# Performance work log

Hardware: AMD Instinct MI355X
Metric: run time of the kernel (lower is better)

Reference implementation:

```python
import jax, jax.numpy as jnp
import numpy as np

# Dimensions
B, T, S, V, CV, D = 32, 128, 400, 32000, 600, 512
PAD = 1  # vocabs['code'].stoi['<blank>']


def setup_inputs() -> dict:
    key = jax.random.key(0)
    k0, k1, k2, k3, k4 = jax.random.split(key, 5)
    hidden = jax.random.normal(k0, (B * T, D), dtype=jnp.float32)
    # attention weights: normalized over source length
    copy_attn = jax.nn.softmax(jax.random.normal(k1, (B * T, S), dtype=jnp.float32), axis=-1)
    # src_map: one-hot scatter matrix [B, S, CV] mapping src positions to extended-vocab ids
    src_ids = jax.random.randint(k2, (B, S), 0, CV)
    src_map = jax.nn.one_hot(src_ids, CV, dtype=jnp.float32)
    W = jax.random.normal(k3, (V, D), dtype=jnp.float32) * 0.02
    b = jnp.zeros((V,), dtype=jnp.float32)
    w_copy = jax.random.normal(k4, (D,), dtype=jnp.float32) * 0.02
    b_copy = jnp.zeros((), dtype=jnp.float32)
    return {"hidden": hidden, "copy_attn": copy_attn, "src_map": src_map,
            "W": W, "b": b, "w_copy": w_copy, "b_copy": b_copy}


def reference(hidden, copy_attn, src_map, W, b, w_copy, b_copy):
    # logits over target vocab, pad logit masked to -inf
    logits = hidden @ W.T + b                      # [B*T, V]
    logits = logits.at[:, PAD].set(-jnp.inf)
    prob = jax.nn.softmax(logits, axis=-1)         # [B*T, V]
    # copy gate p(z)
    copy = jax.nn.sigmoid(hidden @ w_copy + b_copy)[:, None]  # [B*T, 1]
    out_prob = prob * (1.0 - copy)                 # generation branch
    mul_attn = copy_attn * copy                    # copy branch, [B*T, S]
    # scatter attention mass into extended vocab via one-hot bmm
    copy_prob = jnp.einsum('bts,bsv->btv', mul_attn.reshape(B, T, S), src_map)
    copy_prob = copy_prob.reshape(-1, src_map.shape[-1])  # [B*T, CV]
    return jnp.concatenate([out_prob, copy_prob], axis=1)  # [B*T, V+CV]
```

## Files before the change

kernel.cpp:

```cpp
#include <hip/hip_runtime.h>
#include <hip/hip_bf16.h>
#include <cstdint>
#include <cstddef>

#define M_ROWS   4096
#define N_VOCAB  32000
#define K_DIM    512
#define S_DIM    400
#define CV_DIM   600
#define OUT_PITCH 32600
#define PAD_IDX  1

typedef __attribute__((ext_vector_type(8))) short short8;
typedef __attribute__((ext_vector_type(8))) unsigned short ushort8;
typedef __attribute__((ext_vector_type(4))) float f32x4;

#define WB_OFF   0ull
#define HB_OFF   32768000ull
#define COPYG_OFF 36962304ull
#define RSUM_OFF  36978688ull
#define SSCALE_OFF 36995072ull
#define SRCID_OFF 37011456ull
#define EB_OFF    37062656ull
#define WS_NEED_BF16 (EB_OFF + 262144000ull)

__device__ inline void gload_lds16(const void* g, void* l) {
  __builtin_amdgcn_global_load_lds(
      (const __attribute__((address_space(1))) unsigned int*)g,
      (__attribute__((address_space(3))) unsigned int*)l, 16, 0, 0);
}

__device__ inline unsigned short f32_to_bf16_rn(float f) {
  unsigned u = __float_as_uint(f);
  u += 0x7FFFu + ((u >> 16) & 1u);
  return (unsigned short)(u >> 16);
}
__device__ inline float bf16_to_f32(unsigned short h) {
  return __uint_as_float((unsigned)h << 16);
}

__global__ void cvt_kernel(const float4* __restrict__ in, ushort4* __restrict__ out, unsigned n4) {
  unsigned stride = gridDim.x * blockDim.x;
  for (unsigned i = blockIdx.x * blockDim.x + threadIdx.x; i < n4; i += stride) {
    float4 v = in[i];
    ushort4 o;
    o.x = f32_to_bf16_rn(v.x);
    o.y = f32_to_bf16_rn(v.y);
    o.z = f32_to_bf16_rn(v.z);
    o.w = f32_to_bf16_rn(v.w);
    out[i] = o;
  }
}

__global__ void copygate_cvt_kernel(const float* __restrict__ hidden,
                                    const float* __restrict__ w_copy,
                                    const float* __restrict__ b_copy,
                                    float* __restrict__ copyg,
                                    unsigned short* __restrict__ Hb) {
  unsigned gw = (blockIdx.x * blockDim.x + threadIdx.x) >> 6;
  unsigned lane = threadIdx.x & 63u;
  if (gw >= M_ROWS) return;
  const float4* h4 = (const float4*)(hidden + (size_t)gw * K_DIM);
  const float4* w4 = (const float4*)w_copy;
  float4 a0 = h4[lane * 2 + 0], w0 = w4[lane * 2 + 0];
  float4 a1 = h4[lane * 2 + 1], w1 = w4[lane * 2 + 1];
  float dot = a0.x * w0.x + a0.y * w0.y + a0.z * w0.z + a0.w * w0.w
            + a1.x * w1.x + a1.y * w1.y + a1.z * w1.z + a1.w * w1.w;
  ushort8 hb;
  hb[0] = f32_to_bf16_rn(a0.x); hb[1] = f32_to_bf16_rn(a0.y);
  hb[2] = f32_to_bf16_rn(a0.z); hb[3] = f32_to_bf16_rn(a0.w);
  hb[4] = f32_to_bf16_rn(a1.x); hb[5] = f32_to_bf16_rn(a1.y);
  hb[6] = f32_to_bf16_rn(a1.z); hb[7] = f32_to_bf16_rn(a1.w);
  *(ushort8*)(Hb + (size_t)gw * K_DIM + lane * 8u) = hb;
  #pragma unroll
  for (int mask = 1; mask < 64; mask <<= 1) dot += __shfl_xor(dot, mask);
  if (lane == 0) copyg[gw] = 1.f / (1.f + __expf(-(dot + b_copy[0])));
}

__global__ void srcids_kernel(const float* __restrict__ src_map, int* __restrict__ src_ids) {
  unsigned pos = (blockIdx.x * blockDim.x + threadIdx.x) >> 6;
  unsigned lane = threadIdx.x & 63u;
  if (pos >= 32 * S_DIM) return;
  const float* row = src_map + (size_t)pos * CV_DIM;
  int found = 1 << 30;
  for (int v = lane; v < CV_DIM; v += 64)
    if (row[v] > 0.5f) found = v;
  #pragma unroll
  for (int mask = 1; mask < 64; mask <<= 1) {
    int o = __shfl_xor(found, mask);
    found = found < o ? found : o;
  }
  if (lane == 0) src_ids[pos] = found;
}

template<int BF16OUT>
__global__ __launch_bounds__(512, 2)
void gemm_exp_kernel(const unsigned short* __restrict__ A,
                     const unsigned short* __restrict__ B,
                     const float* __restrict__ bias,
                     float* __restrict__ out,
                     unsigned short* __restrict__ Eb,
                     float* __restrict__ row_sum) {
  __shared__ unsigned short smem[24576];
  unsigned short* As = smem;
  unsigned short* Bs = smem + 16384;

  unsigned bid = blockIdx.x;
  unsigned xcd = bid & 7u, local = bid >> 3;
  unsigned slab = xcd >> 1, half = xcd & 1u;
  unsigned nt = half * 125u + (local >> 2);
  unsigned mt = slab * 4u + (local & 3u);
  unsigned m0 = mt * 256u, n0 = nt * 128u;

  unsigned tid = threadIdx.x;
  unsigned lane = tid & 63u;
  unsigned wid = tid >> 6;
  unsigned wm = wid >> 1, wn = wid & 1u;
  unsigned lr = lane >> 4, lc = lane & 15u;

  const unsigned ch0 = (lr ^ (lc & 7u)) * 8u;
  const unsigned ch1 = ((lr + 4u) ^ (lc & 7u)) * 8u;

  const unsigned short* Asrc[4];
  const unsigned short* Bsrc[2];
  unsigned dstA[4], dstB[2];
  #pragma unroll
  for (unsigned i = 0; i < 4; ++i) {
    unsigned u = i * 512u + tid;
    unsigned rr = u >> 3;
    unsigned ch = (u & 7u) ^ (rr & 7u);
    dstA[i] = u * 16u;
    Asrc[i] = A + (size_t)(m0 + rr) * K_DIM + ch * 8u;
  }
  #pragma unroll
  for (unsigned i = 0; i < 2; ++i) {
    unsigned u = i * 512u + tid;
    unsigned rr = u >> 3;
    unsigned ch = (u & 7u) ^ (rr & 7u);
    dstB[i] = u * 16u;
    Bsrc[i] = B + (size_t)(n0 + rr) * K_DIM + ch * 8u;
  }
  unsigned arow[4], brow[4];
  #pragma unroll
  for (int m = 0; m < 4; ++m) arow[m] = (wm * 64u + m * 16u + lc) * 64u;
  #pragma unroll
  for (int n = 0; n < 4; ++n) brow[n] = 16384u + (wn * 64u + n * 16u + lc) * 64u;

  f32x4 acc[4][4] = {};

  for (unsigned kt = 0; kt < 8; ++kt) {
    unsigned k0 = kt * 64u;
    #pragma unroll
    for (unsigned i = 0; i < 4; ++i)
      gload_lds16(Asrc[i] + k0, (char*)As + dstA[i]);
    #pragma unroll
    for (unsigned i = 0; i < 2; ++i)
      gload_lds16(Bsrc[i] + k0, (char*)smem + 32768u + dstB[i]);
    __syncthreads();
    {
      short8 af[4][2], bf[4][2];
      #pragma unroll
      for (int m = 0; m < 4; ++m) {
        af[m][0] = *(const short8*)&As[arow[m] + ch0];
        af[m][1] = *(const short8*)&As[arow[m] + ch1];
      }
      #pragma unroll
      for (int n = 0; n < 4; ++n) {
        bf[n][0] = *(const short8*)&smem[brow[n] + ch0];
        bf[n][1] = *(const short8*)&smem[brow[n] + ch1];
      }
      #pragma unroll
      for (int ks = 0; ks < 2; ++ks)
        #pragma unroll
        for (int m = 0; m < 4; ++m)
          #pragma unroll
          for (int n = 0; n < 4; ++n)
            acc[m][n] = __builtin_amdgcn_mfma_f32_16x16x32_bf16(bf[n][ks], af[m][ks],
                                                                acc[m][n], 0, 0, 0);
    }
    __syncthreads();
  }

  float4 bv4[4];
  #pragma unroll
  for (int n = 0; n < 4; ++n)
    bv4[n] = *(const float4*)&bias[n0 + wn * 64u + n * 16u + lr * 4u];

  if (BF16OUT) {
    #pragma unroll
    for (int m = 0; m < 4; ++m) {
      unsigned grow = m0 + wm * 64u + m * 16u + lc;
      unsigned short* rowp = Eb + (size_t)grow * N_VOCAB;
      #pragma unroll
      for (int n = 0; n < 4; ++n) {
        unsigned gcol = n0 + wn * 64u + n * 16u + lr * 4u;
        float e0 = (gcol + 0u == PAD_IDX) ? 0.f : __expf(acc[m][n][0] + bv4[n].x);
        float e1 = (gcol + 1u == PAD_IDX) ? 0.f : __expf(acc[m][n][1] + bv4[n].y);
        float e2 = (gcol + 2u == PAD_IDX) ? 0.f : __expf(acc[m][n][2] + bv4[n].z);
        float e3 = (gcol + 3u == PAD_IDX) ? 0.f : __expf(acc[m][n][3] + bv4[n].w);
        ushort4 o;
        o.x = f32_to_bf16_rn(e0); o.y = f32_to_bf16_rn(e1);
        o.z = f32_to_bf16_rn(e2); o.w = f32_to_bf16_rn(e3);
        *(ushort4*)(rowp + gcol) = o;
      }
    }
  } else {
    #pragma unroll
    for (int m = 0; m < 4; ++m) {
      unsigned grow = m0 + wm * 64u + m * 16u + lc;
      float rs = 0.f;
      #pragma unroll
      for (int n = 0; n < 4; ++n) {
        unsigned gcol = n0 + wn * 64u + n * 16u + lr * 4u;
        float4 e;
        e.x = (gcol + 0u == PAD_IDX) ? 0.f : __expf(acc[m][n][0] + bv4[n].x);
        e.y = (gcol + 1u == PAD_IDX) ? 0.f : __expf(acc[m][n][1] + bv4[n].y);
        e.z = (gcol + 2u == PAD_IDX) ? 0.f : __expf(acc[m][n][2] + bv4[n].z);
        e.w = (gcol + 3u == PAD_IDX) ? 0.f : __expf(acc[m][n][3] + bv4[n].w);
        *(float4*)(out + (size_t)grow * OUT_PITCH + gcol) = e;
        rs += e.x + e.y + e.z + e.w;
      }
      rs += __shfl_xor(rs, 16);
      rs += __shfl_xor(rs, 32);
      if (lr == 0) atomicAdd(&row_sum[grow], rs);
    }
  }
}

__global__ __launch_bounds__(256)
void norm_scale_kernel(const unsigned short* __restrict__ Eb,
                       const float* __restrict__ copyg,
                       float* __restrict__ out) {
  unsigned r = blockIdx.x;
  unsigned tid = threadIdx.x;
  const ushort8* src = (const ushort8*)(Eb + (size_t)r * N_VOCAB);
  ushort8 v[16];
  float lsum = 0.f;
  #pragma unroll
  for (int i = 0; i < 16; ++i) {
    unsigned c = (unsigned)i * 256u + tid;
    if (c < 4000u) {
      v[i] = src[c];
      #pragma unroll
      for (int k = 0; k < 8; ++k) lsum += bf16_to_f32(v[i][k]);
    }
  }
  #pragma unroll
  for (int mask = 1; mask < 64; mask <<= 1) lsum += __shfl_xor(lsum, mask);
  __shared__ float wsum[4];
  if ((tid & 63u) == 0) wsum[tid >> 6] = lsum;
  __syncthreads();
  float s = (1.f - copyg[r]) / (wsum[0] + wsum[1] + wsum[2] + wsum[3]);
  float* dst = out + (size_t)r * OUT_PITCH;
  #pragma unroll
  for (int i = 0; i < 16; ++i) {
    unsigned c = (unsigned)i * 256u + tid;
    if (c < 4000u) {
      float4 lo, hi;
      lo.x = bf16_to_f32(v[i][0]) * s; lo.y = bf16_to_f32(v[i][1]) * s;
      lo.z = bf16_to_f32(v[i][2]) * s; lo.w = bf16_to_f32(v[i][3]) * s;
      hi.x = bf16_to_f32(v[i][4]) * s; hi.y = bf16_to_f32(v[i][5]) * s;
      hi.z = bf16_to_f32(v[i][6]) * s; hi.w = bf16_to_f32(v[i][7]) * s;
      float4* o = (float4*)(dst + c * 8u);
      o[0] = lo; o[1] = hi;
    }
  }
}

__global__ void finalize_kernel(const float* __restrict__ row_sum, const float* __restrict__ copyg,
                                float* __restrict__ sscale) {
  unsigned r = blockIdx.x * blockDim.x + threadIdx.x;
  if (r < M_ROWS) sscale[r] = (1.f - copyg[r]) / row_sum[r];
}

__global__ void scale_kernel(float4* __restrict__ out, const float* __restrict__ sscale) {
  const unsigned total = M_ROWS * (N_VOCAB / 4);
  unsigned stride = gridDim.x * blockDim.x;
  for (unsigned i = blockIdx.x * blockDim.x + threadIdx.x; i < total; i += stride) {
    unsigned r = i / (N_VOCAB / 4);
    unsigned c = i % (N_VOCAB / 4);
    float s = sscale[r];
    float4 v = out[(size_t)r * (OUT_PITCH / 4) + c];
    v.x *= s; v.y *= s; v.z *= s; v.w *= s;
    out[(size_t)r * (OUT_PITCH / 4) + c] = v;
  }
}

__global__ void copyprob_kernel(const float* __restrict__ attn, const int* __restrict__ src_ids,
                                const float* __restrict__ copyg, float* __restrict__ out) {
  unsigned r = blockIdx.x;
  unsigned tid = threadIdx.x;
  __shared__ float cp[CV_DIM];
  for (unsigned v = tid; v < CV_DIM; v += 128) cp[v] = 0.f;
  __syncthreads();
  unsigned batch = r >> 7;
  float g = copyg[r];
  for (unsigned s = tid; s < S_DIM; s += 128) {
    float a = attn[(size_t)r * S_DIM + s] * g;
    atomicAdd(&cp[src_ids[batch * S_DIM + s]], a);
  }
  __syncthreads();
  for (unsigned v = tid; v < CV_DIM; v += 128)
    out[(size_t)r * OUT_PITCH + N_VOCAB + v] = cp[v];
}

extern "C" void kernel_launch(void* const* d_in, const int* in_sizes, int n_in,
                              void* d_out, int out_size, void* d_ws, size_t ws_size,
                              hipStream_t stream) {
  const float* hidden    = (const float*)d_in[0];
  const float* copy_attn = (const float*)d_in[1];
  const float* src_map   = (const float*)d_in[2];
  const float* W         = (const float*)d_in[3];
  const float* bias      = (const float*)d_in[4];
  const float* w_copy    = (const float*)d_in[5];
  const float* b_copy    = (const float*)d_in[6];
  float* out = (float*)d_out;

  char* ws = (char*)d_ws;
  unsigned short* Wb = (unsigned short*)(ws + WB_OFF);
  unsigned short* Hb = (unsigned short*)(ws + HB_OFF);
  float* copyg   = (float*)(ws + COPYG_OFF);
  float* row_sum = (float*)(ws + RSUM_OFF);
  float* sscale  = (float*)(ws + SSCALE_OFF);
  int*   src_ids = (int*)(ws + SRCID_OFF);
  unsigned short* Eb = (unsigned short*)(ws + EB_OFF);

  const bool bf16_path = (ws_size >= WS_NEED_BF16);

  cvt_kernel<<<2048, 256, 0, stream>>>((const float4*)W, (ushort4*)Wb,
                                       (unsigned)(N_VOCAB * K_DIM / 4));
  copygate_cvt_kernel<<<M_ROWS / 4, 256, 0, stream>>>(hidden, w_copy, b_copy, copyg, Hb);
  srcids_kernel<<<(32 * S_DIM) / 4, 256, 0, stream>>>(src_map, src_ids);

  if (bf16_path) {
    gemm_exp_kernel<1><<<(M_ROWS / 256) * (N_VOCAB / 128), 512, 0, stream>>>(
        Hb, Wb, bias, out, Eb, row_sum);
    norm_scale_kernel<<<M_ROWS, 256, 0, stream>>>(Eb, copyg, out);
  } else {
    hipMemsetAsync(row_sum, 0, M_ROWS * sizeof(float), stream);
    gemm_exp_kernel<0><<<(M_ROWS / 256) * (N_VOCAB / 128), 512, 0, stream>>>(
        Hb, Wb, bias, out, Eb, row_sum);
    finalize_kernel<<<(M_ROWS + 255) / 256, 256, 0, stream>>>(row_sum, copyg, sscale);
    scale_kernel<<<4096, 256, 0, stream>>>((float4*)out, sscale);
  }

  copyprob_kernel<<<M_ROWS, 128, 0, stream>>>(copy_attn, src_ids, copyg, out);
}
```

Baseline: 410.5 us.

## Switch logits GEMM operands from bf16 to fp8 e4m3 with fp8 MFMA

Hidden and W are quantized to fp8 e4m3 instead of bf16, and the GEMM uses the 16x16x32 fp8 MFMA with 128-wide K tiles, which halves the number of K iterations and the operand bytes moved. The shared-memory layout and fragment addressing are reworked for 8-byte fp8 fragments, keeping the XOR swizzle. This cuts conversion traffic, GEMM load bandwidth and MFMA count. The cost is a large loss of precision in the logits (fp8 with no scaling), which may exceed the output tolerance after the softmax exponential.

```diff
diff --git a/kernel.cpp b/kernel.cpp
--- a/kernel.cpp
+++ b/kernel.cpp
@@ -1,5 +1,6 @@
 #include <hip/hip_runtime.h>
 #include <hip/hip_bf16.h>
+#include <hip/hip_fp8.h>
 #include <cstdint>
 #include <cstddef>
 
@@ -14,15 +15,16 @@
 typedef __attribute__((ext_vector_type(8))) short short8;
 typedef __attribute__((ext_vector_type(8))) unsigned short ushort8;
 typedef __attribute__((ext_vector_type(4))) float f32x4;
-
-#define WB_OFF   0ull
-#define HB_OFF   32768000ull
-#define COPYG_OFF 36962304ull
-#define RSUM_OFF  36978688ull
-#define SSCALE_OFF 36995072ull
-#define SRCID_OFF 37011456ull
-#define EB_OFF    37062656ull
-#define WS_NEED_BF16 (EB_OFF + 262144000ull)
+typedef long long i64;
+
+#define W8_OFF   0ull
+#define H8_OFF   16384000ull
+#define COPYG_OFF 18481152ull
+#define RSUM_OFF  18497536ull
+#define SSCALE_OFF 18513920ull
+#define SRCID_OFF 18530304ull
+#define EB_OFF    18581504ull
+#define WS_NEED   (EB_OFF + 262144000ull)
 
 __device__ inline void gload_lds16(const void* g, void* l) {
   __builtin_amdgcn_global_load_lds(
@@ -38,17 +40,17 @@
 __device__ inline float bf16_to_f32(unsigned short h) {
   return __uint_as_float((unsigned)h << 16);
 }
-
-__global__ void cvt_kernel(const float4* __restrict__ in, ushort4* __restrict__ out, unsigned n4) {
+__device__ inline unsigned f32_to_fp8(float f) {
+  __hip_fp8_e4m3 q(f);
+  return (unsigned)(unsigned char)q.__x;
+}
+
+__global__ void cvt8_kernel(const float4* __restrict__ in, unsigned* __restrict__ out, unsigned n4) {
   unsigned stride = gridDim.x * blockDim.x;
   for (unsigned i = blockIdx.x * blockDim.x + threadIdx.x; i < n4; i += stride) {
     float4 v = in[i];
-    ushort4 o;
-    o.x = f32_to_bf16_rn(v.x);
-    o.y = f32_to_bf16_rn(v.y);
-    o.z = f32_to_bf16_rn(v.z);
-    o.w = f32_to_bf16_rn(v.w);
-    out[i] = o;
+    out[i] = f32_to_fp8(v.x) | (f32_to_fp8(v.y) << 8)
+           | (f32_to_fp8(v.z) << 16) | (f32_to_fp8(v.w) << 24);
   }
 }
 
@@ -56,7 +58,7 @@
                                     const float* __restrict__ w_copy,
                                     const float* __restrict__ b_copy,
                                     float* __restrict__ copyg,
-                                    unsigned short* __restrict__ Hb) {
+                                    unsigned char* __restrict__ H8) {
   unsigned gw = (blockIdx.x * blockDim.x + threadIdx.x) >> 6;
   unsigned lane = threadIdx.x & 63u;
   if (gw >= M_ROWS) return;
@@ -66,12 +68,12 @@
   float4 a1 = h4[lane * 2 + 1], w1 = w4[lane * 2 + 1];
   float dot = a0.x * w0.x + a0.y * w0.y + a0.z * w0.z + a0.w * w0.w
             + a1.x * w1.x + a1.y * w1.y + a1.z * w1.z + a1.w * w1.w;
-  ushort8 hb;
-  hb[0] = f32_to_bf16_rn(a0.x); hb[1] = f32_to_bf16_rn(a0.y);
-  hb[2] = f32_to_bf16_rn(a0.z); hb[3] = f32_to_bf16_rn(a0.w);
-  hb[4] = f32_to_bf16_rn(a1.x); hb[5] = f32_to_bf16_rn(a1.y);
-  hb[6] = f32_to_bf16_rn(a1.z); hb[7] = f32_to_bf16_rn(a1.w);
-  *(ushort8*)(Hb + (size_t)gw * K_DIM + lane * 8u) = hb;
+  unsigned lo = f32_to_fp8(a0.x) | (f32_to_fp8(a0.y) << 8)
+              | (f32_to_fp8(a0.z) << 16) | (f32_to_fp8(a0.w) << 24);
+  unsigned hi = f32_to_fp8(a1.x) | (f32_to_fp8(a1.y) << 8)
+              | (f32_to_fp8(a1.z) << 16) | (f32_to_fp8(a1.w) << 24);
+  uint2 pk; pk.x = lo; pk.y = hi;
+  *(uint2*)(H8 + (size_t)gw * K_DIM + lane * 8u) = pk;
   #pragma unroll
   for (int mask = 1; mask < 64; mask <<= 1) dot += __shfl_xor(dot, mask);
   if (lane == 0) copyg[gw] = 1.f / (1.f + __expf(-(dot + b_copy[0])));
@@ -95,15 +97,15 @@
 
 template<int BF16OUT>
 __global__ __launch_bounds__(512, 2)
-void gemm_exp_kernel(const unsigned short* __restrict__ A,
-                     const unsigned short* __restrict__ B,
+void gemm_exp_kernel(const unsigned char* __restrict__ A,
+                     const unsigned char* __restrict__ B,
                      const float* __restrict__ bias,
                      float* __restrict__ out,
                      unsigned short* __restrict__ Eb,
                      float* __restrict__ row_sum) {
-  __shared__ unsigned short smem[24576];
-  unsigned short* As = smem;
-  unsigned short* Bs = smem + 16384;
+  __shared__ unsigned char smem[49152];
+  unsigned char* As = smem;
+  unsigned char* Bs = smem + 32768;
 
   unsigned bid = blockIdx.x;
   unsigned xcd = bid & 7u, local = bid >> 3;
@@ -118,11 +120,8 @@
   unsigned wm = wid >> 1, wn = wid & 1u;
   unsigned lr = lane >> 4, lc = lane & 15u;
 
-  const unsigned ch0 = (lr ^ (lc & 7u)) * 8u;
-  const unsigned ch1 = ((lr + 4u) ^ (lc & 7u)) * 8u;
-
-  const unsigned short* Asrc[4];
-  const unsigned short* Bsrc[2];
+  const unsigned char* Asrc[4];
+  const unsigned char* Bsrc[2];
   unsigned dstA[4], dstB[2];
   #pragma unroll
   for (unsigned i = 0; i < 4; ++i) {
@@ -130,7 +129,7 @@
     unsigned rr = u >> 3;
     unsigned ch = (u & 7u) ^ (rr & 7u);
     dstA[i] = u * 16u;
-    Asrc[i] = A + (size_t)(m0 + rr) * K_DIM + ch * 8u;
+    Asrc[i] = A + (size_t)(m0 + rr) * K_DIM + ch * 16u;
   }
   #pragma unroll
   for (unsigned i = 0; i < 2; ++i) {
@@ -138,45 +137,48 @@
     unsigned rr = u >> 3;
     unsigned ch = (u & 7u) ^ (rr & 7u);
     dstB[i] = u * 16u;
-    Bsrc[i] = B + (size_t)(n0 + rr) * K_DIM + ch * 8u;
-  }
-  unsigned arow[4], brow[4];
-  #pragma unroll
-  for (int m = 0; m < 4; ++m) arow[m] = (wm * 64u + m * 16u + lc) * 64u;
-  #pragma unroll
-  for (int n = 0; n < 4; ++n) brow[n] = 16384u + (wn * 64u + n * 16u + lc) * 64u;
+    Bsrc[i] = B + (size_t)(n0 + rr) * K_DIM + ch * 16u;
+  }
+  unsigned abase[4], akey[4], bbase[4], bkey[4];
+  #pragma unroll
+  for (int m = 0; m < 4; ++m) {
+    unsigned r = wm * 64u + m * 16u + lc;
+    abase[m] = r * 128u; akey[m] = r & 7u;
+  }
+  #pragma unroll
+  for (int n = 0; n < 4; ++n) {
+    unsigned r = wn * 64u + n * 16u + lc;
+    bbase[n] = r * 128u; bkey[n] = r & 7u;
+  }
+  const unsigned hsel = (lr & 1u) * 8u;
 
   f32x4 acc[4][4] = {};
 
-  for (unsigned kt = 0; kt < 8; ++kt) {
-    unsigned k0 = kt * 64u;
+  for (unsigned kt = 0; kt < 4; ++kt) {
+    unsigned k0 = kt * 128u;
     #pragma unroll
     for (unsigned i = 0; i < 4; ++i)
-      gload_lds16(Asrc[i] + k0, (char*)As + dstA[i]);
+      gload_lds16(Asrc[i] + k0, As + dstA[i]);
     #pragma unroll
     for (unsigned i = 0; i < 2; ++i)
-      gload_lds16(Bsrc[i] + k0, (char*)smem + 32768u + dstB[i]);
+      gload_lds16(Bsrc[i] + k0, Bs + dstB[i]);
     __syncthreads();
-    {
-      short8 af[4][2], bf[4][2];
-      #pragma unroll
-      for (int m = 0; m < 4; ++m) {
-        af[m][0] = *(const short8*)&As[arow[m] + ch0];
-        af[m][1] = *(const short8*)&As[arow[m] + ch1];
-      }
-      #pragma unroll
-      for (int n = 0; n < 4; ++n) {
-        bf[n][0] = *(const short8*)&smem[brow[n] + ch0];
-        bf[n][1] = *(const short8*)&smem[brow[n] + ch1];
-      }
-      #pragma unroll
-      for (int ks = 0; ks < 2; ++ks)
+    #pragma unroll
+    for (unsigned ks = 0; ks < 4; ++ks) {
+      unsigned h = ks * 2u + (lr >> 1);
+      i64 av[4], bv[4];
+      #pragma unroll
+      for (int m = 0; m < 4; ++m)
+        av[m] = *(const i64*)(As + abase[m] + ((h ^ akey[m]) * 16u) + hsel);
+      #pragma unroll
+      for (int n = 0; n < 4; ++n)
+        bv[n] = *(const i64*)(Bs + bbase[n] + ((h ^ bkey[n]) * 16u) + hsel);
+      #pragma unroll
+      for (int m = 0; m < 4; ++m)
         #pragma unroll
-        for (int m = 0; m < 4; ++m)
-          #pragma unroll
-          for (int n = 0; n < 4; ++n)
-            acc[m][n] = __builtin_amdgcn_mfma_f32_16x16x32_bf16(bf[n][ks], af[m][ks],
-                                                                acc[m][n], 0, 0, 0);
+        for (int n = 0; n < 4; ++n)
+          acc[m][n] = __builtin_amdgcn_mfma_f32_16x16x32_fp8_fp8(bv[n], av[m],
+                                                                 acc[m][n], 0, 0, 0);
     }
     __syncthreads();
   }
@@ -317,29 +319,29 @@
   float* out = (float*)d_out;
 
   char* ws = (char*)d_ws;
-  unsigned short* Wb = (unsigned short*)(ws + WB_OFF);
-  unsigned short* Hb = (unsigned short*)(ws + HB_OFF);
+  unsigned char* W8 = (unsigned char*)(ws + W8_OFF);
+  unsigned char* H8 = (unsigned char*)(ws + H8_OFF);
   float* copyg   = (float*)(ws + COPYG_OFF);
   float* row_sum = (float*)(ws + RSUM_OFF);
   float* sscale  = (float*)(ws + SSCALE_OFF);
   int*   src_ids = (int*)(ws + SRCID_OFF);
   unsigned short* Eb = (unsigned short*)(ws + EB_OFF);
 
-  const bool bf16_path = (ws_size >= WS_NEED_BF16);
-
-  cvt_kernel<<<2048, 256, 0, stream>>>((const float4*)W, (ushort4*)Wb,
-                                       (unsigned)(N_VOCAB * K_DIM / 4));
-  copygate_cvt_kernel<<<M_ROWS / 4, 256, 0, stream>>>(hidden, w_copy, b_copy, copyg, Hb);
+  const bool bf16_path = (ws_size >= WS_NEED);
+
+  cvt8_kernel<<<2048, 256, 0, stream>>>((const float4*)W, (unsigned*)W8,
+                                        (unsigned)(N_VOCAB * K_DIM / 4));
+  copygate_cvt_kernel<<<M_ROWS / 4, 256, 0, stream>>>(hidden, w_copy, b_copy, copyg, H8);
   srcids_kernel<<<(32 * S_DIM) / 4, 256, 0, stream>>>(src_map, src_ids);
 
   if (bf16_path) {
     gemm_exp_kernel<1><<<(M_ROWS / 256) * (N_VOCAB / 128), 512, 0, stream>>>(
-        Hb, Wb, bias, out, Eb, row_sum);
+        H8, W8, bias, out, Eb, row_sum);
     norm_scale_kernel<<<M_ROWS, 256, 0, stream>>>(Eb, copyg, out);
   } else {
     hipMemsetAsync(row_sum, 0, M_ROWS * sizeof(float), stream);
     gemm_exp_kernel<0><<<(M_ROWS / 256) * (N_VOCAB / 128), 512, 0, stream>>>(
-        Hb, Wb, bias, out, Eb, row_sum);
+        H8, W8, bias, out, Eb, row_sum);
     finalize_kernel<<<(M_ROWS + 255) / 256, 256, 0, stream>>>(row_sum, copyg, sscale);
     scale_kernel<<<4096, 256, 0, stream>>>((float4*)out, sscale);
   }
```

Result: faster. 363.5 us (-11.4%).
